# Kernel tuning notes

Hardware: AMD Instinct MI355X
Metric: run time of the kernel (lower is better)

Reference implementation:

```python
import jax, jax.numpy as jnp
import numpy as np

LN_EPS = 1e-5  # torch LayerNorm default


def layer_norm(x, g, b):
    m = jnp.mean(x, axis=-1, keepdims=True)
    v = jnp.mean((x - m) ** 2, axis=-1, keepdims=True)
    return (x - m) / jnp.sqrt(v + LN_EPS) * g + b


def scatter_mean(src, idx, n):
    # src: [E, h], idx: [E] -> [n, h], mean with count clamped to >= 1
    s = jax.ops.segment_sum(src, idx, num_segments=n)
    cnt = jax.ops.segment_sum(jnp.ones((src.shape[0],), src.dtype), idx, num_segments=n)
    return s / jnp.clip(cnt, 1.0)[:, None]


def setup_inputs() -> dict:
    key = jax.random.key(0)
    ks = jax.random.split(key, 16)
    N, C, E, h = 200000, 50000, 600000, 128

    def w(k, shape, fan_in):
        return (jax.random.normal(k, shape, jnp.float32) / np.float32(np.sqrt(fan_in)))

    ci = jax.random.randint(ks[2], (E,), 0, C)
    vi = jax.random.randint(ks[3], (E,), 0, N)
    return {
        "vh": jax.random.normal(ks[0], (N, h), jnp.float32),
        "ch": jax.random.normal(ks[1], (C, h), jnp.float32),
        "edge_index": jnp.stack([ci, vi]).astype(jnp.int64),
        "ew": jax.random.normal(ks[4], (E,), jnp.float32),
        "v2c_lin_w": w(ks[5], (h, h), h), "v2c_lin_b": jnp.zeros((h,), jnp.float32),
        "v2c_gate_w": w(ks[6], (h, 1), 1), "v2c_gate_b": jnp.zeros((h,), jnp.float32),
        "v2c_upd_w": w(ks[7], (h, 2 * h), 2 * h), "v2c_upd_b": jnp.zeros((h,), jnp.float32),
        "v2c_ln_g": jnp.ones((h,), jnp.float32), "v2c_ln_b": jnp.zeros((h,), jnp.float32),
        "c2v_lin_w": w(ks[8], (h, h), h), "c2v_lin_b": jnp.zeros((h,), jnp.float32),
        "c2v_gate_w": w(ks[9], (h, 1), 1), "c2v_gate_b": jnp.zeros((h,), jnp.float32),
        "c2v_upd_w": w(ks[10], (h, 2 * h), 2 * h), "c2v_upd_b": jnp.zeros((h,), jnp.float32),
        "c2v_ln_g": jnp.ones((h,), jnp.float32), "c2v_ln_b": jnp.zeros((h,), jnp.float32),
    }


def reference(vh, ch, edge_index, ew,
              v2c_lin_w, v2c_lin_b, v2c_gate_w, v2c_gate_b,
              v2c_upd_w, v2c_upd_b, v2c_ln_g, v2c_ln_b,
              c2v_lin_w, c2v_lin_b, c2v_gate_w, c2v_gate_b,
              c2v_upd_w, c2v_upd_b, c2v_ln_g, c2v_ln_b):
    ci, vi = edge_index[0], edge_index[1]
    e = ew[:, None]  # [E, 1]

    # var -> con
    gate = jax.nn.sigmoid(e @ v2c_gate_w.T + v2c_gate_b)          # [E, h]
    msg = (vh @ v2c_lin_w.T + v2c_lin_b)[vi] * gate               # gather + gate
    agg = scatter_mean(msg, ci, ch.shape[0])                      # [C, h]
    ch_new = jax.nn.relu(layer_norm(
        jnp.concatenate([agg, ch], -1) @ v2c_upd_w.T + v2c_upd_b,
        v2c_ln_g, v2c_ln_b))

    # con -> var (uses updated ch)
    gate = jax.nn.sigmoid(e @ c2v_gate_w.T + c2v_gate_b)
    msg = (ch_new @ c2v_lin_w.T + c2v_lin_b)[ci] * gate
    agg = scatter_mean(msg, vi, vh.shape[0])                      # [N, h]
    vh_new = jax.nn.relu(layer_norm(
        jnp.concatenate([agg, vh], -1) @ c2v_upd_w.T + c2v_upd_b,
        c2v_ln_g, c2v_ln_b))

    return vh_new, ch_new
```

## Files before the change

### kernel.cpp

```cpp
#include <hip/hip_runtime.h>

#define LN_EPS 1e-5f

typedef float f32x4 __attribute__((ext_vector_type(4)));
typedef short bf16x8 __attribute__((ext_vector_type(8)));
typedef unsigned short u16x4 __attribute__((ext_vector_type(4)));

__device__ __forceinline__ unsigned short f2bf(float f) {
  unsigned int u = __float_as_uint(f);
  u = (u + 0x7fffu + ((u >> 16) & 1u)) >> 16;
  return (unsigned short)u;
}
__device__ __forceinline__ float bf2f(unsigned short h) {
  return __uint_as_float((unsigned int)h << 16);
}
__device__ __forceinline__ float sigm(float x) {
  return 1.f / (1.f + __expf(-x));
}

__global__ __launch_bounds__(256) void cvt_hist(const float* __restrict__ wa,
                                                const float* __restrict__ wb,
                                                const float* __restrict__ wc,
                                                const float* __restrict__ wd,
                                                unsigned short* __restrict__ oa,
                                                unsigned short* __restrict__ ob,
                                                unsigned short* __restrict__ oc,
                                                unsigned short* __restrict__ od,
                                                const int* __restrict__ ci,
                                                const int* __restrict__ vi,
                                                int* __restrict__ cntC,
                                                int* __restrict__ cntV,
                                                int* __restrict__ rankC,
                                                int* __restrict__ rankV, int E, int hgrid) {
  if ((int)blockIdx.x < 384) {
    int i = blockIdx.x * 256 + threadIdx.x;
    if (i < 16384) oa[i] = f2bf(wa[i]);
    else if (i < 49152) ob[i - 16384] = f2bf(wb[i - 16384]);
    else if (i < 65536) oc[i - 49152] = f2bf(wc[i - 49152]);
    else if (i < 98304) od[i - 65536] = f2bf(wd[i - 65536]);
    return;
  }
  int hb = blockIdx.x - 384;
  int tid = hb * 256 + threadIdx.x;
  int T = hgrid * 256;
  int e[4], c[4], v[4];
  bool ok[4];
#pragma unroll
  for (int i = 0; i < 4; ++i) {
    e[i] = tid + i * T;
    ok[i] = e[i] < E;
  }
#pragma unroll
  for (int i = 0; i < 4; ++i) if (ok[i]) c[i] = ci[e[i]];
#pragma unroll
  for (int i = 0; i < 4; ++i) if (ok[i]) v[i] = vi[e[i]];
  int rc[4], rv[4];
#pragma unroll
  for (int i = 0; i < 4; ++i) if (ok[i]) rc[i] = atomicAdd(&cntC[c[i]], 1);
#pragma unroll
  for (int i = 0; i < 4; ++i) if (ok[i]) rv[i] = atomicAdd(&cntV[v[i]], 1);
#pragma unroll
  for (int i = 0; i < 4; ++i) if (ok[i]) rankC[e[i]] = rc[i];
#pragma unroll
  for (int i = 0; i < 4; ++i) if (ok[i]) rankV[e[i]] = rv[i];
}

__device__ __forceinline__ void scan1_body(const int* __restrict__ cnt,
                                           int* __restrict__ off,
                                           int* __restrict__ bsum, int M, int bid,
                                           int* s) {
  int base = bid * 1024 + threadIdx.x * 4;
  int v[4];
  int tot = 0;
#pragma unroll
  for (int i = 0; i < 4; ++i) {
    int idx = base + i;
    v[i] = (idx < M) ? cnt[idx] : 0;
    tot += v[i];
  }
  s[threadIdx.x] = tot;
  __syncthreads();
  for (int d = 1; d < 256; d <<= 1) {
    int t = (threadIdx.x >= d) ? s[threadIdx.x - d] : 0;
    __syncthreads();
    s[threadIdx.x] += t;
    __syncthreads();
  }
  int excl = s[threadIdx.x] - tot;
#pragma unroll
  for (int i = 0; i < 4; ++i) {
    int idx = base + i;
    if (idx < M) off[idx] = excl;
    excl += v[i];
  }
  if (threadIdx.x == 255) bsum[bid] = s[255];
}

__global__ __launch_bounds__(256) void scanA(const int* __restrict__ cntC,
                                             int* __restrict__ offC,
                                             int* __restrict__ bsC, int Mc,
                                             const int* __restrict__ cntV,
                                             int* __restrict__ offV,
                                             int* __restrict__ bsV, int Mv, int nbC) {
  __shared__ int s[256];
  if ((int)blockIdx.x < nbC)
    scan1_body(cntC, offC, bsC, Mc, blockIdx.x, s);
  else
    scan1_body(cntV, offV, bsV, Mv, blockIdx.x - nbC, s);
}

__global__ __launch_bounds__(256) void scanB(int* __restrict__ bsC, int nbC,
                                             int* __restrict__ bsV, int nbV) {
  __shared__ int s[256];
  __shared__ int carry;
  int* bsum = (blockIdx.x == 0) ? bsC : bsV;
  int nb = (blockIdx.x == 0) ? nbC : nbV;
  if (threadIdx.x == 0) carry = 0;
  __syncthreads();
  for (int base = 0; base < nb; base += 256) {
    int idx = base + threadIdx.x;
    int v = (idx < nb) ? bsum[idx] : 0;
    s[threadIdx.x] = v;
    __syncthreads();
    for (int d = 1; d < 256; d <<= 1) {
      int t = (threadIdx.x >= d) ? s[threadIdx.x - d] : 0;
      __syncthreads();
      s[threadIdx.x] += t;
      __syncthreads();
    }
    if (idx < nb) bsum[idx] = s[threadIdx.x] - v + carry;
    __syncthreads();
    if (threadIdx.x == 0) carry += s[255];
    __syncthreads();
  }
}

__global__ __launch_bounds__(256) void scanC(int* __restrict__ offC,
                                             const int* __restrict__ bsC, int Mc,
                                             int* __restrict__ offV,
                                             const int* __restrict__ bsV, int Mv,
                                             int E, int gC) {
  if ((int)blockIdx.x < gC) {
    int idx = blockIdx.x * 256 + threadIdx.x;
    if (idx < Mc) offC[idx] += bsC[idx >> 10];
    if (idx == Mc) offC[Mc] = E;
  } else {
    int idx = (blockIdx.x - gC) * 256 + threadIdx.x;
    if (idx < Mv) offV[idx] += bsV[idx >> 10];
    if (idx == Mv) offV[Mv] = E;
  }
}

__global__ __launch_bounds__(512) void lin_scatter(
    const float* __restrict__ X, const unsigned short* __restrict__ Wbf,
    const float* __restrict__ bias, unsigned short* __restrict__ out,
    unsigned short* __restrict__ bfdst, int M,
    const int* __restrict__ ci, const int* __restrict__ vi,
    const float* __restrict__ ew, const int* __restrict__ offC,
    const int* __restrict__ offV, const int* __restrict__ rankC,
    const int* __restrict__ rankV, int2* __restrict__ edataC,
    int2* __restrict__ edataV, int E, int sgrid) {
  __shared__ unsigned short Bs[128][136];
  const int tid = threadIdx.x;

  if ((int)blockIdx.x < sgrid) {
    int gtid = blockIdx.x * 512 + tid;
    int T = sgrid * 512;
    int e[2], c[2], v[2], wb[2], rc[2], rv[2];
    bool ok[2];
#pragma unroll
    for (int i = 0; i < 2; ++i) {
      e[i] = gtid + i * T;
      ok[i] = e[i] < E;
    }
#pragma unroll
    for (int i = 0; i < 2; ++i) if (ok[i]) c[i] = ci[e[i]];
#pragma unroll
    for (int i = 0; i < 2; ++i) if (ok[i]) v[i] = vi[e[i]];
#pragma unroll
    for (int i = 0; i < 2; ++i) if (ok[i]) wb[i] = __float_as_int(ew[e[i]]);
#pragma unroll
    for (int i = 0; i < 2; ++i) if (ok[i]) rc[i] = rankC[e[i]];
#pragma unroll
    for (int i = 0; i < 2; ++i) if (ok[i]) rv[i] = rankV[e[i]];
#pragma unroll
    for (int i = 0; i < 2; ++i) if (ok[i]) edataC[offC[c[i]] + rc[i]] = make_int2(v[i], wb[i]);
#pragma unroll
    for (int i = 0; i < 2; ++i) if (ok[i]) edataV[offV[v[i]] + rv[i]] = make_int2(c[i], wb[i]);
    return;
  }

  const int bid = blockIdx.x - sgrid;
  const int lane = tid & 63, wv = tid >> 6;
  const int lr = lane & 15, lg = lane >> 4;
  const int row0 = bid * 128 + wv * 16;
  const int arow = row0 + lr;
  const bool rowok = arow < M;
  const float* xrow = X + (size_t)arow * 128;

  float4 x0[4], x1[4];
#pragma unroll
  for (int ks = 0; ks < 4; ++ks) {
    int kb = ks * 32 + lg * 8;
    if (rowok) {
      x0[ks] = *reinterpret_cast<const float4*>(xrow + kb);
      x1[ks] = *reinterpret_cast<const float4*>(xrow + kb + 4);
    } else {
      x0[ks] = make_float4(0.f, 0.f, 0.f, 0.f);
      x1[ks] = x0[ks];
    }
  }

#pragma unroll
  for (int it = 0; it < 4; ++it) {
    int q = tid + it * 512;
    int n = q >> 4, kq = (q & 15) * 8;
    *reinterpret_cast<bf16x8*>(&Bs[n][kq]) =
        *reinterpret_cast<const bf16x8*>(&Wbf[(size_t)n * 128 + kq]);
  }

  bf16x8 a[4];
#pragma unroll
  for (int ks = 0; ks < 4; ++ks) {
    a[ks] = (bf16x8){(short)f2bf(x0[ks].x), (short)f2bf(x0[ks].y),
                     (short)f2bf(x0[ks].z), (short)f2bf(x0[ks].w),
                     (short)f2bf(x1[ks].x), (short)f2bf(x1[ks].y),
                     (short)f2bf(x1[ks].z), (short)f2bf(x1[ks].w)};
    if (rowok)
      *reinterpret_cast<bf16x8*>(&bfdst[(size_t)arow * 256 + 128 + ks * 32 + lg * 8]) = a[ks];
  }
  __syncthreads();

  f32x4 acc[8];
#pragma unroll
  for (int nf = 0; nf < 8; ++nf) acc[nf] = (f32x4)(0.f);
#pragma unroll
  for (int ks = 0; ks < 4; ++ks) {
#pragma unroll
    for (int nf = 0; nf < 8; ++nf) {
      bf16x8 b = *reinterpret_cast<const bf16x8*>(&Bs[nf * 16 + lr][ks * 32 + lg * 8]);
      acc[nf] = __builtin_amdgcn_mfma_f32_16x16x32_bf16(a[ks], b, acc[nf], 0, 0, 0);
    }
  }

#pragma unroll
  for (int nf = 0; nf < 8; ++nf) {
    int col = nf * 16 + lr;
    float bv = bias[col];
#pragma unroll
    for (int reg = 0; reg < 4; ++reg) {
      int grow = row0 + lg * 4 + reg;
      if (grow < M) out[(size_t)grow * 256 + col] = f2bf(acc[nf][reg] + bv);
    }
  }
}

__global__ __launch_bounds__(256) void seg_reduce(const int* __restrict__ off,
                                                  const int2* __restrict__ edata,
                                                  const float* __restrict__ gw,
                                                  const float* __restrict__ gb,
                                                  const unsigned short* __restrict__ src,
                                                  int srcStride,
                                                  unsigned short* __restrict__ out,
                                                  int outStride, int M) {
  int seg = blockIdx.x * 4 + (threadIdx.x >> 6);
  if (seg >= M) return;
  int j = threadIdx.x & 63;
  int start = off[seg], end = off[seg + 1];
  float gwa = gw[2 * j], gwb = gw[2 * j + 1];
  float gba = gb[2 * j], gbb = gb[2 * j + 1];
  float a0 = 0.f, a1 = 0.f;
  int p = start;
  for (; p + 4 <= end; p += 4) {
    int2 e0 = edata[p], e1 = edata[p + 1], e2 = edata[p + 2], e3 = edata[p + 3];
    unsigned int v0 = *reinterpret_cast<const unsigned int*>(&src[(size_t)e0.x * srcStride + 2 * j]);
    unsigned int v1 = *reinterpret_cast<const unsigned int*>(&src[(size_t)e1.x * srcStride + 2 * j]);
    unsigned int v2 = *reinterpret_cast<const unsigned int*>(&src[(size_t)e2.x * srcStride + 2 * j]);
    unsigned int v3 = *reinterpret_cast<const unsigned int*>(&src[(size_t)e3.x * srcStride + 2 * j]);
    float w0 = __int_as_float(e0.y), w1 = __int_as_float(e1.y);
    float w2 = __int_as_float(e2.y), w3 = __int_as_float(e3.y);
    a0 += bf2f((unsigned short)(v0 & 0xffff)) * sigm(w0 * gwa + gba)
        + bf2f((unsigned short)(v1 & 0xffff)) * sigm(w1 * gwa + gba)
        + bf2f((unsigned short)(v2 & 0xffff)) * sigm(w2 * gwa + gba)
        + bf2f((unsigned short)(v3 & 0xffff)) * sigm(w3 * gwa + gba);
    a1 += bf2f((unsigned short)(v0 >> 16)) * sigm(w0 * gwb + gbb)
        + bf2f((unsigned short)(v1 >> 16)) * sigm(w1 * gwb + gbb)
        + bf2f((unsigned short)(v2 >> 16)) * sigm(w2 * gwb + gbb)
        + bf2f((unsigned short)(v3 >> 16)) * sigm(w3 * gwb + gbb);
  }
  if (p + 2 <= end) {
    int2 e0 = edata[p], e1 = edata[p + 1];
    unsigned int v0 = *reinterpret_cast<const unsigned int*>(&src[(size_t)e0.x * srcStride + 2 * j]);
    unsigned int v1 = *reinterpret_cast<const unsigned int*>(&src[(size_t)e1.x * srcStride + 2 * j]);
    float w0 = __int_as_float(e0.y), w1 = __int_as_float(e1.y);
    a0 += bf2f((unsigned short)(v0 & 0xffff)) * sigm(w0 * gwa + gba)
        + bf2f((unsigned short)(v1 & 0xffff)) * sigm(w1 * gwa + gba);
    a1 += bf2f((unsigned short)(v0 >> 16)) * sigm(w0 * gwb + gbb)
        + bf2f((unsigned short)(v1 >> 16)) * sigm(w1 * gwb + gbb);
    p += 2;
  }
  if (p < end) {
    int2 e0 = edata[p];
    unsigned int v0 = *reinterpret_cast<const unsigned int*>(&src[(size_t)e0.x * srcStride + 2 * j]);
    float w0 = __int_as_float(e0.y);
    a0 += bf2f((unsigned short)(v0 & 0xffff)) * sigm(w0 * gwa + gba);
    a1 += bf2f((unsigned short)(v0 >> 16)) * sigm(w0 * gwb + gbb);
  }
  int cnt = end - start;
  float inv = 1.f / (float)(cnt > 1 ? cnt : 1);
  unsigned int packed = (unsigned int)f2bf(a0 * inv) | ((unsigned int)f2bf(a1 * inv) << 16);
  *reinterpret_cast<unsigned int*>(&out[(size_t)seg * outStride + 2 * j]) = packed;
}

__global__ __launch_bounds__(512) void gemm_lin_reg(const float* __restrict__ X,
                                                    const unsigned short* __restrict__ Wbf,
                                                    const float* __restrict__ bias,
                                                    unsigned short* __restrict__ out,
                                                    int M) {
  __shared__ unsigned short Bs[128][136];
  const int tid = threadIdx.x;
  const int lane = tid & 63, wv = tid >> 6;
  const int lr = lane & 15, lg = lane >> 4;
  const int row0 = blockIdx.x * 128 + wv * 16;
  const int arow = row0 + lr;
  const bool rowok = arow < M;
  const float* xrow = X + (size_t)arow * 128;

  float4 x0[4], x1[4];
#pragma unroll
  for (int ks = 0; ks < 4; ++ks) {
    int kb = ks * 32 + lg * 8;
    if (rowok) {
      x0[ks] = *reinterpret_cast<const float4*>(xrow + kb);
      x1[ks] = *reinterpret_cast<const float4*>(xrow + kb + 4);
    } else {
      x0[ks] = make_float4(0.f, 0.f, 0.f, 0.f);
      x1[ks] = x0[ks];
    }
  }
#pragma unroll
  for (int it = 0; it < 4; ++it) {
    int q = tid + it * 512;
    int n = q >> 4, kq = (q & 15) * 8;
    *reinterpret_cast<bf16x8*>(&Bs[n][kq]) =
        *reinterpret_cast<const bf16x8*>(&Wbf[(size_t)n * 128 + kq]);
  }
  bf16x8 a[4];
#pragma unroll
  for (int ks = 0; ks < 4; ++ks)
    a[ks] = (bf16x8){(short)f2bf(x0[ks].x), (short)f2bf(x0[ks].y),
                     (short)f2bf(x0[ks].z), (short)f2bf(x0[ks].w),
                     (short)f2bf(x1[ks].x), (short)f2bf(x1[ks].y),
                     (short)f2bf(x1[ks].z), (short)f2bf(x1[ks].w)};
  __syncthreads();

  f32x4 acc[8];
#pragma unroll
  for (int nf = 0; nf < 8; ++nf) acc[nf] = (f32x4)(0.f);
#pragma unroll
  for (int ks = 0; ks < 4; ++ks) {
#pragma unroll
    for (int nf = 0; nf < 8; ++nf) {
      bf16x8 b = *reinterpret_cast<const bf16x8*>(&Bs[nf * 16 + lr][ks * 32 + lg * 8]);
      acc[nf] = __builtin_amdgcn_mfma_f32_16x16x32_bf16(a[ks], b, acc[nf], 0, 0, 0);
    }
  }
#pragma unroll
  for (int nf = 0; nf < 8; ++nf) {
    int col = nf * 16 + lr;
    float bv = bias[col];
#pragma unroll
    for (int reg = 0; reg < 4; ++reg) {
      int grow = row0 + lg * 4 + reg;
      if (grow < M) out[(size_t)grow * 128 + col] = f2bf(acc[nf][reg] + bv);
    }
  }
}

template <bool CAT>
__global__ __launch_bounds__(512) void gemm_upd_reg(const unsigned short* __restrict__ Xa,
                                                    const float* __restrict__ base,
                                                    const unsigned short* __restrict__ Wbf,
                                                    const float* __restrict__ bias,
                                                    const float* __restrict__ lng,
                                                    const float* __restrict__ lnb,
                                                    float* __restrict__ out, int M) {
  __shared__ unsigned short Bs[128][136];
  const int tid = threadIdx.x;
  const int lane = tid & 63, wv = tid >> 6;
  const int lr = lane & 15, lg = lane >> 4;
  const int row0 = blockIdx.x * 128 + wv * 16;
  const int arow = row0 + lr;
  const bool rowok = arow < M;

  bf16x8 a[8];
  if constexpr (CAT) {
    const unsigned short* xr = Xa + (size_t)arow * 256;
#pragma unroll
    for (int ks = 0; ks < 8; ++ks)
      a[ks] = rowok ? *reinterpret_cast<const bf16x8*>(xr + ks * 32 + lg * 8) : (bf16x8)(short)0;
  } else {
    const unsigned short* ar = Xa + (size_t)arow * 128;
#pragma unroll
    for (int ks = 0; ks < 4; ++ks)
      a[ks] = rowok ? *reinterpret_cast<const bf16x8*>(ar + ks * 32 + lg * 8) : (bf16x8)(short)0;
    const float* br = base + (size_t)arow * 128;
#pragma unroll
    for (int ks = 4; ks < 8; ++ks) {
      float4 f0 = make_float4(0.f, 0.f, 0.f, 0.f), f1 = f0;
      if (rowok) {
        int kb = (ks - 4) * 32 + lg * 8;
        f0 = *reinterpret_cast<const float4*>(br + kb);
        f1 = *reinterpret_cast<const float4*>(br + kb + 4);
      }
      a[ks] = (bf16x8){(short)f2bf(f0.x), (short)f2bf(f0.y), (short)f2bf(f0.z), (short)f2bf(f0.w),
                       (short)f2bf(f1.x), (short)f2bf(f1.y), (short)f2bf(f1.z), (short)f2bf(f1.w)};
    }
  }

  auto stageW = [&](int kh) {
#pragma unroll
    for (int it = 0; it < 4; ++it) {
      int q = tid + it * 512;
      int n = q >> 4, kq = (q & 15) * 8;
      *reinterpret_cast<bf16x8*>(&Bs[n][kq]) =
          *reinterpret_cast<const bf16x8*>(&Wbf[(size_t)n * 256 + kh * 128 + kq]);
    }
  };

  f32x4 acc[8];
#pragma unroll
  for (int nf = 0; nf < 8; ++nf) acc[nf] = (f32x4)(0.f);

  stageW(0);
  __syncthreads();
#pragma unroll
  for (int ks = 0; ks < 4; ++ks) {
#pragma unroll
    for (int nf = 0; nf < 8; ++nf) {
      bf16x8 b = *reinterpret_cast<const bf16x8*>(&Bs[nf * 16 + lr][ks * 32 + lg * 8]);
      acc[nf] = __builtin_amdgcn_mfma_f32_16x16x32_bf16(a[ks], b, acc[nf], 0, 0, 0);
    }
  }
  __syncthreads();
  stageW(1);
  __syncthreads();
#pragma unroll
  for (int ks = 4; ks < 8; ++ks) {
#pragma unroll
    for (int nf = 0; nf < 8; ++nf) {
      bf16x8 b = *reinterpret_cast<const bf16x8*>(&Bs[nf * 16 + lr][(ks - 4) * 32 + lg * 8]);
      acc[nf] = __builtin_amdgcn_mfma_f32_16x16x32_bf16(a[ks], b, acc[nf], 0, 0, 0);
    }
  }

  float bv[8], gv[8], lv[8];
#pragma unroll
  for (int nf = 0; nf < 8; ++nf) {
    int col = nf * 16 + lr;
    bv[nf] = bias[col];
    gv[nf] = lng[col];
    lv[nf] = lnb[col];
  }
#pragma unroll
  for (int reg = 0; reg < 4; ++reg) {
    float z[8];
    float s = 0.f, q = 0.f;
#pragma unroll
    for (int nf = 0; nf < 8; ++nf) {
      z[nf] = acc[nf][reg] + bv[nf];
      s += z[nf];
      q += z[nf] * z[nf];
    }
#pragma unroll
    for (int m = 1; m < 16; m <<= 1) {
      s += __shfl_xor(s, m);
      q += __shfl_xor(q, m);
    }
    float mean = s * (1.f / 128.f);
    float var = q * (1.f / 128.f) - mean * mean;
    float rstd = rsqrtf(var + LN_EPS);
    int grow = row0 + lg * 4 + reg;
    if (grow < M) {
#pragma unroll
      for (int nf = 0; nf < 8; ++nf) {
        float y = (z[nf] - mean) * rstd * gv[nf] + lv[nf];
        out[(size_t)grow * 128 + nf * 16 + lr] = fmaxf(y, 0.f);
      }
    }
  }
}

extern "C" void kernel_launch(void* const* d_in, const int* in_sizes, int n_in,
                              void* d_out, int out_size, void* d_ws, size_t ws_size,
                              hipStream_t stream) {
  const float* vh = (const float*)d_in[0];
  const float* ch = (const float*)d_in[1];
  const int* ei = (const int*)d_in[2];
  const float* ew = (const float*)d_in[3];
  const float* v2c_lin_w = (const float*)d_in[4];
  const float* v2c_lin_b = (const float*)d_in[5];
  const float* v2c_gate_w = (const float*)d_in[6];
  const float* v2c_gate_b = (const float*)d_in[7];
  const float* v2c_upd_w = (const float*)d_in[8];
  const float* v2c_upd_b = (const float*)d_in[9];
  const float* v2c_ln_g = (const float*)d_in[10];
  const float* v2c_ln_b = (const float*)d_in[11];
  const float* c2v_lin_w = (const float*)d_in[12];
  const float* c2v_lin_b = (const float*)d_in[13];
  const float* c2v_gate_w = (const float*)d_in[14];
  const float* c2v_gate_b = (const float*)d_in[15];
  const float* c2v_upd_w = (const float*)d_in[16];
  const float* c2v_upd_b = (const float*)d_in[17];
  const float* c2v_ln_g = (const float*)d_in[18];
  const float* c2v_ln_b = (const float*)d_in[19];

  const int N = in_sizes[0] / 128;
  const int C = in_sizes[1] / 128;
  const int E = in_sizes[3];
  const int* ci = ei;
  const int* vi = ei + E;

  unsigned short* Xcat = (unsigned short*)d_ws;
  unsigned short* aggC = Xcat + (size_t)N * 256;
  unsigned short* wbf = aggC + (size_t)C * 128;
  unsigned short* wbfLinV = wbf;
  unsigned short* wbfUpdV = wbf + 16384;
  unsigned short* wbfLinC = wbf + 49152;
  unsigned short* wbfUpdC = wbf + 65536;
  int* offC = (int*)(wbf + 98304);
  int* offV = offC + (C + 1);
  size_t ofs = (size_t)((offV + (N + 1)) - (int*)d_ws);
  ofs = (ofs + 1) & ~(size_t)1;
  int2* edataC = (int2*)((int*)d_ws + ofs);
  int2* edataV = edataC + E;
  int* cntC = (int*)aggC;
  int* cntV = cntC + C;
  int* bsumC = cntV + N;
  int* bsumV = bsumC + 512;
  int* rankC = bsumV + 512;
  int* rankV = rankC + E;

  float* vhNew = (float*)d_out;
  float* chNew = (float*)d_out + (size_t)N * 128;

  const int hgrid = (E + 4 * 256 - 1) / (4 * 256);
  const int sgrid = (E + 2 * 512 - 1) / (2 * 512);
  const int nbC = (C + 1023) / 1024;
  const int nbN = (N + 1023) / 1024;
  const int gC = (C + 1 + 255) / 256;
  const int gN = (N + 1 + 255) / 256;

  hipMemsetAsync(cntC, 0, (size_t)(C + N) * sizeof(int), stream);
  cvt_hist<<<384 + hgrid, 256, 0, stream>>>(v2c_lin_w, v2c_upd_w, c2v_lin_w, c2v_upd_w,
                                            wbfLinV, wbfUpdV, wbfLinC, wbfUpdC,
                                            ci, vi, cntC, cntV, rankC, rankV, E, hgrid);

  scanA<<<nbC + nbN, 256, 0, stream>>>(cntC, offC, bsumC, C, cntV, offV, bsumV, N, nbC);
  scanB<<<2, 256, 0, stream>>>(bsumC, nbC, bsumV, nbN);
  scanC<<<gC + gN, 256, 0, stream>>>(offC, bsumC, C, offV, bsumV, N, E, gC);

  lin_scatter<<<sgrid + (N + 127) / 128, 512, 0, stream>>>(
      vh, wbfLinV, v2c_lin_b, Xcat, Xcat, N,
      ci, vi, ew, offC, offV, rankC, rankV, edataC, edataV, E, sgrid);

  seg_reduce<<<(C + 3) / 4, 256, 0, stream>>>(offC, edataC, v2c_gate_w, v2c_gate_b,
                                              Xcat, 256, aggC, 128, C);
  gemm_upd_reg<false><<<(C + 127) / 128, 512, 0, stream>>>(aggC, ch, wbfUpdV, v2c_upd_b,
                                                           v2c_ln_g, v2c_ln_b, chNew, C);

  unsigned short* tmpC = aggC;
  gemm_lin_reg<<<(C + 127) / 128, 512, 0, stream>>>(chNew, wbfLinC, c2v_lin_b, tmpC, C);
  seg_reduce<<<(N + 3) / 4, 256, 0, stream>>>(offV, edataV, c2v_gate_w, c2v_gate_b,
                                              tmpC, 128, Xcat, 256, N);
  gemm_upd_reg<true><<<(N + 127) / 128, 512, 0, stream>>>(Xcat, nullptr, wbfUpdC,
                                                          c2v_upd_b, c2v_ln_g, c2v_ln_b,
                                                          vhNew, N);
}
```

Baseline: 315.6 us.

## Use persistent grid-stride blocks for GEMM and segment-reduce kernels

Converts the GEMM kernels and segment reduction to persistent grid-stride loops with fixed grid sizes. Each block stages the bf16 weights into LDS once and reuses them across many row tiles. The update GEMM now stages the full 256-wide K weight at once, which drops the mid-kernel resync and restage. This cuts repeated weight loads and block launch overhead, but the larger LDS footprint and fixed grids may lower occupancy and latency hiding for the gather-bound reduction.

```diff
diff --git a/kernel.cpp b/kernel.cpp
--- a/kernel.cpp
+++ b/kernel.cpp
@@ -159,7 +159,7 @@
     const float* __restrict__ ew, const int* __restrict__ offC,
     const int* __restrict__ offV, const int* __restrict__ rankC,
     const int* __restrict__ rankV, int2* __restrict__ edataC,
-    int2* __restrict__ edataV, int E, int sgrid) {
+    int2* __restrict__ edataV, int E, int sgrid, int lgrid) {
   __shared__ unsigned short Bs[128][136];
   const int tid = threadIdx.x;
 
@@ -193,23 +193,6 @@
   const int bid = blockIdx.x - sgrid;
   const int lane = tid & 63, wv = tid >> 6;
   const int lr = lane & 15, lg = lane >> 4;
-  const int row0 = bid * 128 + wv * 16;
-  const int arow = row0 + lr;
-  const bool rowok = arow < M;
-  const float* xrow = X + (size_t)arow * 128;
-
-  float4 x0[4], x1[4];
-#pragma unroll
-  for (int ks = 0; ks < 4; ++ks) {
-    int kb = ks * 32 + lg * 8;
-    if (rowok) {
-      x0[ks] = *reinterpret_cast<const float4*>(xrow + kb);
-      x1[ks] = *reinterpret_cast<const float4*>(xrow + kb + 4);
-    } else {
-      x0[ks] = make_float4(0.f, 0.f, 0.f, 0.f);
-      x1[ks] = x0[ks];
-    }
-  }
 
 #pragma unroll
   for (int it = 0; it < 4; ++it) {
@@ -218,39 +201,127 @@
     *reinterpret_cast<bf16x8*>(&Bs[n][kq]) =
         *reinterpret_cast<const bf16x8*>(&Wbf[(size_t)n * 128 + kq]);
   }
-
-  bf16x8 a[4];
-#pragma unroll
-  for (int ks = 0; ks < 4; ++ks) {
-    a[ks] = (bf16x8){(short)f2bf(x0[ks].x), (short)f2bf(x0[ks].y),
-                     (short)f2bf(x0[ks].z), (short)f2bf(x0[ks].w),
-                     (short)f2bf(x1[ks].x), (short)f2bf(x1[ks].y),
-                     (short)f2bf(x1[ks].z), (short)f2bf(x1[ks].w)};
-    if (rowok)
-      *reinterpret_cast<bf16x8*>(&bfdst[(size_t)arow * 256 + 128 + ks * 32 + lg * 8]) = a[ks];
-  }
   __syncthreads();
 
-  f32x4 acc[8];
-#pragma unroll
-  for (int nf = 0; nf < 8; ++nf) acc[nf] = (f32x4)(0.f);
-#pragma unroll
-  for (int ks = 0; ks < 4; ++ks) {
+  const int ntiles = (M + 127) / 128;
+  for (int tile = bid; tile < ntiles; tile += lgrid) {
+    const int row0 = tile * 128 + wv * 16;
+    const int arow = row0 + lr;
+    const bool rowok = arow < M;
+    const float* xrow = X + (size_t)arow * 128;
+
+    float4 x0[4], x1[4];
+#pragma unroll
+    for (int ks = 0; ks < 4; ++ks) {
+      int kb = ks * 32 + lg * 8;
+      if (rowok) {
+        x0[ks] = *reinterpret_cast<const float4*>(xrow + kb);
+        x1[ks] = *reinterpret_cast<const float4*>(xrow + kb + 4);
+      } else {
+        x0[ks] = make_float4(0.f, 0.f, 0.f, 0.f);
+        x1[ks] = x0[ks];
+      }
+    }
+    bf16x8 a[4];
+#pragma unroll
+    for (int ks = 0; ks < 4; ++ks) {
+      a[ks] = (bf16x8){(short)f2bf(x0[ks].x), (short)f2bf(x0[ks].y),
+                       (short)f2bf(x0[ks].z), (short)f2bf(x0[ks].w),
+                       (short)f2bf(x1[ks].x), (short)f2bf(x1[ks].y),
+                       (short)f2bf(x1[ks].z), (short)f2bf(x1[ks].w)};
+      if (rowok)
+        *reinterpret_cast<bf16x8*>(&bfdst[(size_t)arow * 256 + 128 + ks * 32 + lg * 8]) = a[ks];
+    }
+
+    f32x4 acc[8];
+#pragma unroll
+    for (int nf = 0; nf < 8; ++nf) acc[nf] = (f32x4)(0.f);
+#pragma unroll
+    for (int ks = 0; ks < 4; ++ks) {
+#pragma unroll
+      for (int nf = 0; nf < 8; ++nf) {
+        bf16x8 b = *reinterpret_cast<const bf16x8*>(&Bs[nf * 16 + lr][ks * 32 + lg * 8]);
+        acc[nf] = __builtin_amdgcn_mfma_f32_16x16x32_bf16(a[ks], b, acc[nf], 0, 0, 0);
+      }
+    }
 #pragma unroll
     for (int nf = 0; nf < 8; ++nf) {
-      bf16x8 b = *reinterpret_cast<const bf16x8*>(&Bs[nf * 16 + lr][ks * 32 + lg * 8]);
-      acc[nf] = __builtin_amdgcn_mfma_f32_16x16x32_bf16(a[ks], b, acc[nf], 0, 0, 0);
-    }
-  }
-
-#pragma unroll
-  for (int nf = 0; nf < 8; ++nf) {
-    int col = nf * 16 + lr;
-    float bv = bias[col];
-#pragma unroll
-    for (int reg = 0; reg < 4; ++reg) {
-      int grow = row0 + lg * 4 + reg;
-      if (grow < M) out[(size_t)grow * 256 + col] = f2bf(acc[nf][reg] + bv);
+      int col = nf * 16 + lr;
+      float bv = bias[col];
+#pragma unroll
+      for (int reg = 0; reg < 4; ++reg) {
+        int grow = row0 + lg * 4 + reg;
+        if (grow < M) out[(size_t)grow * 256 + col] = f2bf(acc[nf][reg] + bv);
+      }
+    }
+  }
+}
+
+__global__ __launch_bounds__(512) void gemm_lin_reg(const float* __restrict__ X,
+                                                    const unsigned short* __restrict__ Wbf,
+                                                    const float* __restrict__ bias,
+                                                    unsigned short* __restrict__ out,
+                                                    int M, int lgrid) {
+  __shared__ unsigned short Bs[128][136];
+  const int tid = threadIdx.x;
+  const int lane = tid & 63, wv = tid >> 6;
+  const int lr = lane & 15, lg = lane >> 4;
+#pragma unroll
+  for (int it = 0; it < 4; ++it) {
+    int q = tid + it * 512;
+    int n = q >> 4, kq = (q & 15) * 8;
+    *reinterpret_cast<bf16x8*>(&Bs[n][kq]) =
+        *reinterpret_cast<const bf16x8*>(&Wbf[(size_t)n * 128 + kq]);
+  }
+  __syncthreads();
+
+  const int ntiles = (M + 127) / 128;
+  for (int tile = blockIdx.x; tile < ntiles; tile += lgrid) {
+    const int row0 = tile * 128 + wv * 16;
+    const int arow = row0 + lr;
+    const bool rowok = arow < M;
+    const float* xrow = X + (size_t)arow * 128;
+
+    float4 x0[4], x1[4];
+#pragma unroll
+    for (int ks = 0; ks < 4; ++ks) {
+      int kb = ks * 32 + lg * 8;
+      if (rowok) {
+        x0[ks] = *reinterpret_cast<const float4*>(xrow + kb);
+        x1[ks] = *reinterpret_cast<const float4*>(xrow + kb + 4);
+      } else {
+        x0[ks] = make_float4(0.f, 0.f, 0.f, 0.f);
+        x1[ks] = x0[ks];
+      }
+    }
+    bf16x8 a[4];
+#pragma unroll
+    for (int ks = 0; ks < 4; ++ks)
+      a[ks] = (bf16x8){(short)f2bf(x0[ks].x), (short)f2bf(x0[ks].y),
+                       (short)f2bf(x0[ks].z), (short)f2bf(x0[ks].w),
+                       (short)f2bf(x1[ks].x), (short)f2bf(x1[ks].y),
+                       (short)f2bf(x1[ks].z), (short)f2bf(x1[ks].w)};
+
+    f32x4 acc[8];
+#pragma unroll
+    for (int nf = 0; nf < 8; ++nf) acc[nf] = (f32x4)(0.f);
+#pragma unroll
+    for (int ks = 0; ks < 4; ++ks) {
+#pragma unroll
+      for (int nf = 0; nf < 8; ++nf) {
+        bf16x8 b = *reinterpret_cast<const bf16x8*>(&Bs[nf * 16 + lr][ks * 32 + lg * 8]);
+        acc[nf] = __builtin_amdgcn_mfma_f32_16x16x32_bf16(a[ks], b, acc[nf], 0, 0, 0);
+      }
+    }
+#pragma unroll
+    for (int nf = 0; nf < 8; ++nf) {
+      int col = nf * 16 + lr;
+      float bv = bias[col];
+#pragma unroll
+      for (int reg = 0; reg < 4; ++reg) {
+        int grow = row0 + lg * 4 + reg;
+        if (grow < M) out[(size_t)grow * 128 + col] = f2bf(acc[nf][reg] + bv);
+      }
     }
   }
 }
@@ -263,117 +334,53 @@
                                                   int srcStride,
                                                   unsigned short* __restrict__ out,
                                                   int outStride, int M) {
-  int seg = blockIdx.x * 4 + (threadIdx.x >> 6);
-  if (seg >= M) return;
   int j = threadIdx.x & 63;
-  int start = off[seg], end = off[seg + 1];
   float gwa = gw[2 * j], gwb = gw[2 * j + 1];
   float gba = gb[2 * j], gbb = gb[2 * j + 1];
-  float a0 = 0.f, a1 = 0.f;
-  int p = start;
-  for (; p + 4 <= end; p += 4) {
-    int2 e0 = edata[p], e1 = edata[p + 1], e2 = edata[p + 2], e3 = edata[p + 3];
-    unsigned int v0 = *reinterpret_cast<const unsigned int*>(&src[(size_t)e0.x * srcStride + 2 * j]);
-    unsigned int v1 = *reinterpret_cast<const unsigned int*>(&src[(size_t)e1.x * srcStride + 2 * j]);
-    unsigned int v2 = *reinterpret_cast<const unsigned int*>(&src[(size_t)e2.x * srcStride + 2 * j]);
-    unsigned int v3 = *reinterpret_cast<const unsigned int*>(&src[(size_t)e3.x * srcStride + 2 * j]);
-    float w0 = __int_as_float(e0.y), w1 = __int_as_float(e1.y);
-    float w2 = __int_as_float(e2.y), w3 = __int_as_float(e3.y);
-    a0 += bf2f((unsigned short)(v0 & 0xffff)) * sigm(w0 * gwa + gba)
-        + bf2f((unsigned short)(v1 & 0xffff)) * sigm(w1 * gwa + gba)
-        + bf2f((unsigned short)(v2 & 0xffff)) * sigm(w2 * gwa + gba)
-        + bf2f((unsigned short)(v3 & 0xffff)) * sigm(w3 * gwa + gba);
-    a1 += bf2f((unsigned short)(v0 >> 16)) * sigm(w0 * gwb + gbb)
-        + bf2f((unsigned short)(v1 >> 16)) * sigm(w1 * gwb + gbb)
-        + bf2f((unsigned short)(v2 >> 16)) * sigm(w2 * gwb + gbb)
-        + bf2f((unsigned short)(v3 >> 16)) * sigm(w3 * gwb + gbb);
-  }
-  if (p + 2 <= end) {
-    int2 e0 = edata[p], e1 = edata[p + 1];
-    unsigned int v0 = *reinterpret_cast<const unsigned int*>(&src[(size_t)e0.x * srcStride + 2 * j]);
-    unsigned int v1 = *reinterpret_cast<const unsigned int*>(&src[(size_t)e1.x * srcStride + 2 * j]);
-    float w0 = __int_as_float(e0.y), w1 = __int_as_float(e1.y);
-    a0 += bf2f((unsigned short)(v0 & 0xffff)) * sigm(w0 * gwa + gba)
-        + bf2f((unsigned short)(v1 & 0xffff)) * sigm(w1 * gwa + gba);
-    a1 += bf2f((unsigned short)(v0 >> 16)) * sigm(w0 * gwb + gbb)
-        + bf2f((unsigned short)(v1 >> 16)) * sigm(w1 * gwb + gbb);
-    p += 2;
-  }
-  if (p < end) {
-    int2 e0 = edata[p];
-    unsigned int v0 = *reinterpret_cast<const unsigned int*>(&src[(size_t)e0.x * srcStride + 2 * j]);
-    float w0 = __int_as_float(e0.y);
-    a0 += bf2f((unsigned short)(v0 & 0xffff)) * sigm(w0 * gwa + gba);
-    a1 += bf2f((unsigned short)(v0 >> 16)) * sigm(w0 * gwb + gbb);
-  }
-  int cnt = end - start;
-  float inv = 1.f / (float)(cnt > 1 ? cnt : 1);
-  unsigned int packed = (unsigned int)f2bf(a0 * inv) | ((unsigned int)f2bf(a1 * inv) << 16);
-  *reinterpret_cast<unsigned int*>(&out[(size_t)seg * outStride + 2 * j]) = packed;
-}
-
-__global__ __launch_bounds__(512) void gemm_lin_reg(const float* __restrict__ X,
-                                                    const unsigned short* __restrict__ Wbf,
-                                                    const float* __restrict__ bias,
-                                                    unsigned short* __restrict__ out,
-                                                    int M) {
-  __shared__ unsigned short Bs[128][136];
-  const int tid = threadIdx.x;
-  const int lane = tid & 63, wv = tid >> 6;
-  const int lr = lane & 15, lg = lane >> 4;
-  const int row0 = blockIdx.x * 128 + wv * 16;
-  const int arow = row0 + lr;
-  const bool rowok = arow < M;
-  const float* xrow = X + (size_t)arow * 128;
-
-  float4 x0[4], x1[4];
-#pragma unroll
-  for (int ks = 0; ks < 4; ++ks) {
-    int kb = ks * 32 + lg * 8;
-    if (rowok) {
-      x0[ks] = *reinterpret_cast<const float4*>(xrow + kb);
-      x1[ks] = *reinterpret_cast<const float4*>(xrow + kb + 4);
-    } else {
-      x0[ks] = make_float4(0.f, 0.f, 0.f, 0.f);
-      x1[ks] = x0[ks];
-    }
-  }
-#pragma unroll
-  for (int it = 0; it < 4; ++it) {
-    int q = tid + it * 512;
-    int n = q >> 4, kq = (q & 15) * 8;
-    *reinterpret_cast<bf16x8*>(&Bs[n][kq]) =
-        *reinterpret_cast<const bf16x8*>(&Wbf[(size_t)n * 128 + kq]);
-  }
-  bf16x8 a[4];
-#pragma unroll
-  for (int ks = 0; ks < 4; ++ks)
-    a[ks] = (bf16x8){(short)f2bf(x0[ks].x), (short)f2bf(x0[ks].y),
-                     (short)f2bf(x0[ks].z), (short)f2bf(x0[ks].w),
-                     (short)f2bf(x1[ks].x), (short)f2bf(x1[ks].y),
-                     (short)f2bf(x1[ks].z), (short)f2bf(x1[ks].w)};
-  __syncthreads();
-
-  f32x4 acc[8];
-#pragma unroll
-  for (int nf = 0; nf < 8; ++nf) acc[nf] = (f32x4)(0.f);
-#pragma unroll
-  for (int ks = 0; ks < 4; ++ks) {
-#pragma unroll
-    for (int nf = 0; nf < 8; ++nf) {
-      bf16x8 b = *reinterpret_cast<const bf16x8*>(&Bs[nf * 16 + lr][ks * 32 + lg * 8]);
-      acc[nf] = __builtin_amdgcn_mfma_f32_16x16x32_bf16(a[ks], b, acc[nf], 0, 0, 0);
-    }
-  }
-#pragma unroll
-  for (int nf = 0; nf < 8; ++nf) {
-    int col = nf * 16 + lr;
-    float bv = bias[col];
-#pragma unroll
-    for (int reg = 0; reg < 4; ++reg) {
-      int grow = row0 + lg * 4 + reg;
-      if (grow < M) out[(size_t)grow * 128 + col] = f2bf(acc[nf][reg] + bv);
-    }
+  int nwaves = gridDim.x * 4;
+  for (int seg = blockIdx.x * 4 + (threadIdx.x >> 6); seg < M; seg += nwaves) {
+    int start = off[seg], end = off[seg + 1];
+    float a0 = 0.f, a1 = 0.f;
+    int p = start;
+    for (; p + 4 <= end; p += 4) {
+      int2 e0 = edata[p], e1 = edata[p + 1], e2 = edata[p + 2], e3 = edata[p + 3];
+      unsigned int v0 = *reinterpret_cast<const unsigned int*>(&src[(size_t)e0.x * srcStride + 2 * j]);
+      unsigned int v1 = *reinterpret_cast<const unsigned int*>(&src[(size_t)e1.x * srcStride + 2 * j]);
+      unsigned int v2 = *reinterpret_cast<const unsigned int*>(&src[(size_t)e2.x * srcStride + 2 * j]);
+      unsigned int v3 = *reinterpret_cast<const unsigned int*>(&src[(size_t)e3.x * srcStride + 2 * j]);
+      float w0 = __int_as_float(e0.y), w1 = __int_as_float(e1.y);
+      float w2 = __int_as_float(e2.y), w3 = __int_as_float(e3.y);
+      a0 += bf2f((unsigned short)(v0 & 0xffff)) * sigm(w0 * gwa + gba)
+          + bf2f((unsigned short)(v1 & 0xffff)) * sigm(w1 * gwa + gba)
+          + bf2f((unsigned short)(v2 & 0xffff)) * sigm(w2 * gwa + gba)
+          + bf2f((unsigned short)(v3 & 0xffff)) * sigm(w3 * gwa + gba);
+      a1 += bf2f((unsigned short)(v0 >> 16)) * sigm(w0 * gwb + gbb)
+          + bf2f((unsigned short)(v1 >> 16)) * sigm(w1 * gwb + gbb)
+          + bf2f((unsigned short)(v2 >> 16)) * sigm(w2 * gwb + gbb)
+          + bf2f((unsigned short)(v3 >> 16)) * sigm(w3 * gwb + gbb);
+    }
+    if (p + 2 <= end) {
+      int2 e0 = edata[p], e1 = edata[p + 1];
+      unsigned int v0 = *reinterpret_cast<const unsigned int*>(&src[(size_t)e0.x * srcStride + 2 * j]);
+      unsigned int v1 = *reinterpret_cast<const unsigned int*>(&src[(size_t)e1.x * srcStride + 2 * j]);
+      float w0 = __int_as_float(e0.y), w1 = __int_as_float(e1.y);
+      a0 += bf2f((unsigned short)(v0 & 0xffff)) * sigm(w0 * gwa + gba)
+          + bf2f((unsigned short)(v1 & 0xffff)) * sigm(w1 * gwa + gba);
+      a1 += bf2f((unsigned short)(v0 >> 16)) * sigm(w0 * gwb + gbb)
+          + bf2f((unsigned short)(v1 >> 16)) * sigm(w1 * gwb + gbb);
+      p += 2;
+    }
+    if (p < end) {
+      int2 e0 = edata[p];
+      unsigned int v0 = *reinterpret_cast<const unsigned int*>(&src[(size_t)e0.x * srcStride + 2 * j]);
+      float w0 = __int_as_float(e0.y);
+      a0 += bf2f((unsigned short)(v0 & 0xffff)) * sigm(w0 * gwa + gba);
+      a1 += bf2f((unsigned short)(v0 >> 16)) * sigm(w0 * gwb + gbb);
+    }
+    int cnt = end - start;
+    float inv = 1.f / (float)(cnt > 1 ? cnt : 1);
+    unsigned int packed = (unsigned int)f2bf(a0 * inv) | ((unsigned int)f2bf(a1 * inv) << 16);
+    *reinterpret_cast<unsigned int*>(&out[(size_t)seg * outStride + 2 * j]) = packed;
   }
 }
 
@@ -384,75 +391,21 @@
                                                     const float* __restrict__ bias,
                                                     const float* __restrict__ lng,
                                                     const float* __restrict__ lnb,
-                                                    float* __restrict__ out, int M) {
-  __shared__ unsigned short Bs[128][136];
+                                                    float* __restrict__ out, int M,
+                                                    int ugrid) {
+  __shared__ unsigned short Bs[128][264];
   const int tid = threadIdx.x;
   const int lane = tid & 63, wv = tid >> 6;
   const int lr = lane & 15, lg = lane >> 4;
-  const int row0 = blockIdx.x * 128 + wv * 16;
-  const int arow = row0 + lr;
-  const bool rowok = arow < M;
-
-  bf16x8 a[8];
-  if constexpr (CAT) {
-    const unsigned short* xr = Xa + (size_t)arow * 256;
-#pragma unroll
-    for (int ks = 0; ks < 8; ++ks)
-      a[ks] = rowok ? *reinterpret_cast<const bf16x8*>(xr + ks * 32 + lg * 8) : (bf16x8)(short)0;
-  } else {
-    const unsigned short* ar = Xa + (size_t)arow * 128;
-#pragma unroll
-    for (int ks = 0; ks < 4; ++ks)
-      a[ks] = rowok ? *reinterpret_cast<const bf16x8*>(ar + ks * 32 + lg * 8) : (bf16x8)(short)0;
-    const float* br = base + (size_t)arow * 128;
-#pragma unroll
-    for (int ks = 4; ks < 8; ++ks) {
-      float4 f0 = make_float4(0.f, 0.f, 0.f, 0.f), f1 = f0;
-      if (rowok) {
-        int kb = (ks - 4) * 32 + lg * 8;
-        f0 = *reinterpret_cast<const float4*>(br + kb);
-        f1 = *reinterpret_cast<const float4*>(br + kb + 4);
-      }
-      a[ks] = (bf16x8){(short)f2bf(f0.x), (short)f2bf(f0.y), (short)f2bf(f0.z), (short)f2bf(f0.w),
-                       (short)f2bf(f1.x), (short)f2bf(f1.y), (short)f2bf(f1.z), (short)f2bf(f1.w)};
-    }
-  }
-
-  auto stageW = [&](int kh) {
-#pragma unroll
-    for (int it = 0; it < 4; ++it) {
-      int q = tid + it * 512;
-      int n = q >> 4, kq = (q & 15) * 8;
-      *reinterpret_cast<bf16x8*>(&Bs[n][kq]) =
-          *reinterpret_cast<const bf16x8*>(&Wbf[(size_t)n * 256 + kh * 128 + kq]);
-    }
-  };
-
-  f32x4 acc[8];
-#pragma unroll
-  for (int nf = 0; nf < 8; ++nf) acc[nf] = (f32x4)(0.f);
-
-  stageW(0);
+
+#pragma unroll
+  for (int it = 0; it < 8; ++it) {
+    int q = tid + it * 512;
+    int n = q >> 5, kq = (q & 31) * 8;
+    *reinterpret_cast<bf16x8*>(&Bs[n][kq]) =
+        *reinterpret_cast<const bf16x8*>(&Wbf[(size_t)n * 256 + kq]);
+  }
   __syncthreads();
-#pragma unroll
-  for (int ks = 0; ks < 4; ++ks) {
-#pragma unroll
-    for (int nf = 0; nf < 8; ++nf) {
-      bf16x8 b = *reinterpret_cast<const bf16x8*>(&Bs[nf * 16 + lr][ks * 32 + lg * 8]);
-      acc[nf] = __builtin_amdgcn_mfma_f32_16x16x32_bf16(a[ks], b, acc[nf], 0, 0, 0);
-    }
-  }
-  __syncthreads();
-  stageW(1);
-  __syncthreads();
-#pragma unroll
-  for (int ks = 4; ks < 8; ++ks) {
-#pragma unroll
-    for (int nf = 0; nf < 8; ++nf) {
-      bf16x8 b = *reinterpret_cast<const bf16x8*>(&Bs[nf * 16 + lr][(ks - 4) * 32 + lg * 8]);
-      acc[nf] = __builtin_amdgcn_mfma_f32_16x16x32_bf16(a[ks], b, acc[nf], 0, 0, 0);
-    }
-  }
 
   float bv[8], gv[8], lv[8];
 #pragma unroll
@@ -462,30 +415,75 @@
     gv[nf] = lng[col];
     lv[nf] = lnb[col];
   }
-#pragma unroll
-  for (int reg = 0; reg < 4; ++reg) {
-    float z[8];
-    float s = 0.f, q = 0.f;
-#pragma unroll
-    for (int nf = 0; nf < 8; ++nf) {
-      z[nf] = acc[nf][reg] + bv[nf];
-      s += z[nf];
-      q += z[nf] * z[nf];
-    }
-#pragma unroll
-    for (int m = 1; m < 16; m <<= 1) {
-      s += __shfl_xor(s, m);
-      q += __shfl_xor(q, m);
-    }
-    float mean = s * (1.f / 128.f);
-    float var = q * (1.f / 128.f) - mean * mean;
-    float rstd = rsqrtf(var + LN_EPS);
-    int grow = row0 + lg * 4 + reg;
-    if (grow < M) {
+
+  const int ntiles = (M + 127) / 128;
+  for (int tile = blockIdx.x; tile < ntiles; tile += ugrid) {
+    const int row0 = tile * 128 + wv * 16;
+    const int arow = row0 + lr;
+    const bool rowok = arow < M;
+
+    bf16x8 a[8];
+    if constexpr (CAT) {
+      const unsigned short* xr = Xa + (size_t)arow * 256;
+#pragma unroll
+      for (int ks = 0; ks < 8; ++ks)
+        a[ks] = rowok ? *reinterpret_cast<const bf16x8*>(xr + ks * 32 + lg * 8) : (bf16x8)(short)0;
+    } else {
+      const unsigned short* ar = Xa + (size_t)arow * 128;
+#pragma unroll
+      for (int ks = 0; ks < 4; ++ks)
+        a[ks] = rowok ? *reinterpret_cast<const bf16x8*>(ar + ks * 32 + lg * 8) : (bf16x8)(short)0;
+      const float* br = base + (size_t)arow * 128;
+#pragma unroll
+      for (int ks = 4; ks < 8; ++ks) {
+        float4 f0 = make_float4(0.f, 0.f, 0.f, 0.f), f1 = f0;
+        if (rowok) {
+          int kb = (ks - 4) * 32 + lg * 8;
+          f0 = *reinterpret_cast<const float4*>(br + kb);
+          f1 = *reinterpret_cast<const float4*>(br + kb + 4);
+        }
+        a[ks] = (bf16x8){(short)f2bf(f0.x), (short)f2bf(f0.y), (short)f2bf(f0.z), (short)f2bf(f0.w),
+                         (short)f2bf(f1.x), (short)f2bf(f1.y), (short)f2bf(f1.z), (short)f2bf(f1.w)};
+      }
+    }
+
+    f32x4 acc[8];
+#pragma unroll
+    for (int nf = 0; nf < 8; ++nf) acc[nf] = (f32x4)(0.f);
+#pragma unroll
+    for (int ks = 0; ks < 8; ++ks) {
 #pragma unroll
       for (int nf = 0; nf < 8; ++nf) {
-        float y = (z[nf] - mean) * rstd * gv[nf] + lv[nf];
-        out[(size_t)grow * 128 + nf * 16 + lr] = fmaxf(y, 0.f);
+        bf16x8 b = *reinterpret_cast<const bf16x8*>(&Bs[nf * 16 + lr][ks * 32 + lg * 8]);
+        acc[nf] = __builtin_amdgcn_mfma_f32_16x16x32_bf16(a[ks], b, acc[nf], 0, 0, 0);
+      }
+    }
+
+#pragma unroll
+    for (int reg = 0; reg < 4; ++reg) {
+      float z[8];
+      float s = 0.f, q = 0.f;
+#pragma unroll
+      for (int nf = 0; nf < 8; ++nf) {
+        z[nf] = acc[nf][reg] + bv[nf];
+        s += z[nf];
+        q += z[nf] * z[nf];
+      }
+#pragma unroll
+      for (int m = 1; m < 16; m <<= 1) {
+        s += __shfl_xor(s, m);
+        q += __shfl_xor(q, m);
+      }
+      float mean = s * (1.f / 128.f);
+      float var = q * (1.f / 128.f) - mean * mean;
+      float rstd = rsqrtf(var + LN_EPS);
+      int grow = row0 + lg * 4 + reg;
+      if (grow < M) {
+#pragma unroll
+        for (int nf = 0; nf < 8; ++nf) {
+          float y = (z[nf] - mean) * rstd * gv[nf] + lv[nf];
+          out[(size_t)grow * 128 + nf * 16 + lr] = fmaxf(y, 0.f);
+        }
       }
     }
   }
@@ -550,6 +548,9 @@
   const int nbN = (N + 1023) / 1024;
   const int gC = (C + 1 + 255) / 256;
   const int gN = (N + 1 + 255) / 256;
+  const int LGRID = 1024;
+  const int UGRID = 512;
+  const int SEGG = 2048;
 
   hipMemsetAsync(cntC, 0, (size_t)(C + N) * sizeof(int), stream);
   cvt_hist<<<384 + hgrid, 256, 0, stream>>>(v2c_lin_w, v2c_upd_w, c2v_lin_w, c2v_upd_w,
@@ -560,20 +561,20 @@
   scanB<<<2, 256, 0, stream>>>(bsumC, nbC, bsumV, nbN);
   scanC<<<gC + gN, 256, 0, stream>>>(offC, bsumC, C, offV, bsumV, N, E, gC);
 
-  lin_scatter<<<sgrid + (N + 127) / 128, 512, 0, stream>>>(
+  lin_scatter<<<sgrid + LGRID, 512, 0, stream>>>(
       vh, wbfLinV, v2c_lin_b, Xcat, Xcat, N,
-      ci, vi, ew, offC, offV, rankC, rankV, edataC, edataV, E, sgrid);
-
-  seg_reduce<<<(C + 3) / 4, 256, 0, stream>>>(offC, edataC, v2c_gate_w, v2c_gate_b,
-                                              Xcat, 256, aggC, 128, C);
-  gemm_upd_reg<false><<<(C + 127) / 128, 512, 0, stream>>>(aggC, ch, wbfUpdV, v2c_upd_b,
-                                                           v2c_ln_g, v2c_ln_b, chNew, C);
+      ci, vi, ew, offC, offV, rankC, rankV, edataC, edataV, E, sgrid, LGRID);
+
+  seg_reduce<<<SEGG, 256, 0, stream>>>(offC, edataC, v2c_gate_w, v2c_gate_b,
+                                       Xcat, 256, aggC, 128, C);
+  gemm_upd_reg<false><<<UGRID, 512, 0, stream>>>(aggC, ch, wbfUpdV, v2c_upd_b,
+                                                 v2c_ln_g, v2c_ln_b, chNew, C, UGRID);
 
   unsigned short* tmpC = aggC;
-  gemm_lin_reg<<<(C + 127) / 128, 512, 0, stream>>>(chNew, wbfLinC, c2v_lin_b, tmpC, C);
-  seg_reduce<<<(N + 3) / 4, 256, 0, stream>>>(offV, edataV, c2v_gate_w, c2v_gate_b,
-                                              tmpC, 128, Xcat, 256, N);
-  gemm_upd_reg<true><<<(N + 127) / 128, 512, 0, stream>>>(Xcat, nullptr, wbfUpdC,
-                                                          c2v_upd_b, c2v_ln_g, c2v_ln_b,
-                                                          vhNew, N);
-}
+  gemm_lin_reg<<<512, 512, 0, stream>>>(chNew, wbfLinC, c2v_lin_b, tmpC, C, 512);
+  seg_reduce<<<SEGG, 256, 0, stream>>>(offV, edataV, c2v_gate_w, c2v_gate_b,
+                                       tmpC, 128, Xcat, 256, N);
+  gemm_upd_reg<true><<<UGRID, 512, 0, stream>>>(Xcat, nullptr, wbfUpdC,
+                                                c2v_upd_b, c2v_ln_g, c2v_ln_b,
+                                                vhNew, N, UGRID);
+}
```

New measurement: 429.2 us. +36.0%, slower.
